# Kernel tuning notes

Measured on AMD Instinct MI355X. Metric: run time of the kernel, lower is better.

The kernel has to match this reference:

```python
import jax, jax.numpy as jnp
import numpy as np

N = 100000; E = 1600000; F = 128; H = 64; LH = 32; K = 10

def setup_inputs():
    key = jax.random.key(0)
    ks = jax.random.split(key, 26)
    p = lambda k, s: jax.random.normal(k, s, dtype=jnp.float32) * 0.05
    return {
        'x': jax.random.normal(ks[0], (N, F), dtype=jnp.float32),
        'edge_index': jax.random.randint(ks[1], (2, E), 0, N, dtype=jnp.int32),
        'W1': p(ks[2], (F, H)), 'b1': p(ks[3], (H,)),
        'W2': p(ks[4], (H, H)), 'b2': p(ks[5], (H,)),
        'W3': p(ks[6], (H, H)), 'b3': p(ks[7], (H,)),
        'Wih0': p(ks[8], (4 * LH, H)), 'Whh0': p(ks[9], (4 * LH, LH)),
        'bih0': p(ks[10], (4 * LH,)), 'bhh0': p(ks[11], (4 * LH,)),
        'Wih1': p(ks[12], (4 * LH, LH)), 'Whh1': p(ks[13], (4 * LH, LH)),
        'bih1': p(ks[14], (4 * LH,)), 'bhh1': p(ks[15], (4 * LH,)),
        'Wv1': p(ks[16], (LH, H // 2)), 'bv1': p(ks[17], (H // 2,)),
        'Wv2': p(ks[18], (H // 2, 1)), 'bv2': p(ks[19], (1,)),
        'Wt1': p(ks[20], (LH, H // 2)), 'bt1': p(ks[21], (H // 2,)),
        'Wt2': p(ks[22], (H // 2, K)), 'bt2': p(ks[23], (K,)),
    }


def _forward(x, edge_index, W1, b1, W2, b2, W3, b3, Wih0, Whh0, bih0, bhh0, Wih1, Whh1, bih1, bhh1, Wv1, bv1, Wv2, bv2, Wt1, bt1, Wt2, bt2):
    n = x.shape[0]
    loops = jnp.arange(n, dtype=edge_index.dtype)
    # PyG GCNConv default: add self-loops, symmetric normalization
    src = jnp.concatenate([edge_index[0], loops])
    dst = jnp.concatenate([edge_index[1], loops])
    deg = jax.ops.segment_sum(jnp.ones_like(src, dtype=x.dtype), dst, num_segments=n)
    dinv = jnp.where(deg > 0, jax.lax.rsqrt(deg), 0.0)
    norm = (dinv[src] * dinv[dst])[:, None]  # D^-1/2 (A+I) D^-1/2 edge weights

    def gcn(h, W, b):
        h = h @ W                                    # transform first (fewer bytes moved)
        agg = jax.ops.segment_sum(h[src] * norm, dst, num_segments=n)
        return agg + b

    h = jax.nn.relu(gcn(x, W1, b1))   # dropout is identity in eval mode
    h = jax.nn.relu(gcn(h, W2, b2))
    h = jax.nn.relu(gcn(h, W3, b3))

    def lstm_step(inp, Wih, Whh, bih, bhh):
        # seq_len == 1 and h0 = c0 = 0 -> recurrent matmul (Whh @ h0) is zero
        g = inp @ Wih.T + bih + bhh
        i, f, gg, o = jnp.split(g, 4, axis=-1)  # torch gate order: i, f, g, o
        c = jax.nn.sigmoid(i) * jnp.tanh(gg)
        return jax.nn.sigmoid(o) * jnp.tanh(c)

    h = lstm_step(h, Wih0, Whh0, bih0, bhh0)
    h = lstm_step(h, Wih1, Whh1, bih1, bhh1)

    volume_pred = jax.nn.relu(h @ Wv1 + bv1) @ Wv2 + bv2
    type_pred = jax.nn.relu(h @ Wt1 + bt1) @ Wt2 + bt2
    return (volume_pred, type_pred)


def reference(x, edge_index, W1, b1, W2, b2, W3, b3, Wih0, Whh0, bih0, bhh0, Wih1, Whh1, bih1, bhh1, Wv1, bv1, Wv2, bv2, Wt1, bt1, Wt2, bt2):
    return _forward(x, edge_index, W1, b1, W2, b2, W3, b3, Wih0, Whh0, bih0, bhh0, Wih1, Whh1, bih1, bhh1, Wv1, bv1, Wv2, bv2, Wt1, bt1, Wt2, bt2)
```

## Files before the change

### kernel.cpp

```cpp
#include <hip/hip_runtime.h>
#include <math.h>


typedef unsigned int  u32;
typedef unsigned short u16;
typedef short bfrag  __attribute__((ext_vector_type(8)));
typedef float f32x4  __attribute__((ext_vector_type(4)));

#define LOG2E 1.44269504088896f
static __device__ __forceinline__ float fast_sigmoid(float x){
  float t = __builtin_amdgcn_exp2f(-x * LOG2E);
  return __builtin_amdgcn_rcpf(1.f + t);
}
static __device__ __forceinline__ float fast_tanh(float x){
  float t = __builtin_amdgcn_exp2f(x * (2.f * LOG2E));
  return 1.f - 2.f * __builtin_amdgcn_rcpf(t + 1.f);
}
static __device__ __forceinline__ float bf2f(u16 u){ return __uint_as_float(((u32)u)<<16); }
static __device__ __forceinline__ u16   f2bf(float f){
  u32 x = __float_as_uint(f);
  return (u16)((x + 0x7fffu + ((x>>16)&1u)) >> 16);
}

#define MAXBK 512

__global__ __launch_bounds__(512) void bucket_hist_kernel(const int* __restrict__ dstA,
                                                          int* __restrict__ bhist, int E){
  __shared__ int h[MAXBK];
  for (int i=threadIdx.x; i<MAXBK; i+=512) h[i]=0;
  __syncthreads();
  const int base = blockIdx.x*8192;
  #pragma unroll
  for (int j=0;j<16;++j){
    int e = base + j*512 + threadIdx.x;
    if (e < E) atomicAdd(&h[dstA[e]>>8], 1);
  }
  __syncthreads();
  for (int i=threadIdx.x; i<MAXBK; i+=512) if (h[i]) atomicAdd(&bhist[i], h[i]);
}

__global__ __launch_bounds__(512) void bucket_scan_kernel(const int* __restrict__ bhist,
                                                          int* __restrict__ bcur,
                                                          int* __restrict__ bstart){
  __shared__ int ts[MAXBK];
  int v = bhist[threadIdx.x];
  ts[threadIdx.x] = v; __syncthreads();
  for (int off=1; off<MAXBK; off<<=1){
    int t = (threadIdx.x>=off) ? ts[threadIdx.x-off] : 0;
    __syncthreads();
    ts[threadIdx.x] += t;
    __syncthreads();
  }
  int ex = ts[threadIdx.x] - v;
  bcur[threadIdx.x]   = ex;
  bstart[threadIdx.x] = ex;
  if (threadIdx.x == MAXBK-1) bstart[MAXBK] = ts[threadIdx.x];
}

__global__ __launch_bounds__(512) void bin_kernel(const int* __restrict__ srcA,
                                                  const int* __restrict__ dstA,
                                                  int* __restrict__ bcur,
                                                  u32* __restrict__ packed, int E){
  __shared__ int h[MAXBK];
  __shared__ int basev[MAXBK];
  for (int i=threadIdx.x; i<MAXBK; i+=512) h[i]=0;
  __syncthreads();
  const int base = blockIdx.x*8192;
  int br[16]; int dv[16];
  #pragma unroll
  for (int j=0;j<16;++j){
    int e = base + j*512 + threadIdx.x;
    if (e < E){
      int d = dstA[e]; int b = d>>8;
      int r = atomicAdd(&h[b], 1);
      br[j] = (b<<16) | r;
      dv[j] = d;
    } else br[j] = -1;
  }
  __syncthreads();
  for (int i=threadIdx.x; i<MAXBK; i+=512){
    int c = h[i];
    basev[i] = c ? atomicAdd(&bcur[i], c) : 0;
  }
  __syncthreads();
  #pragma unroll
  for (int j=0;j<16;++j){
    if (br[j] >= 0){
      int e = base + j*512 + threadIdx.x;
      int pos = basev[br[j]>>16] + (br[j] & 0xffff);
      packed[pos] = (u32)srcA[e] | ((u32)(dv[j] & 255) << 24);
    }
  }
}

__global__ __launch_bounds__(512) void bucket_finalize_kernel(
    const u32* __restrict__ packed, const int* __restrict__ bstart,
    int* __restrict__ offs, float* __restrict__ dinv,
    int* __restrict__ csr, int n, int E){
  __shared__ int cnt[256];
  __shared__ int sc[256];
  __shared__ int cur[256];
  const int b = blockIdx.x;
  const int start = bstart[b], end = bstart[b+1];
  for (int i=threadIdx.x; i<256; i+=512){ cnt[i]=0; cur[i]=0; }
  __syncthreads();
  for (int e = start + threadIdx.x; e < end; e += 512)
    atomicAdd(&cnt[packed[e] >> 24], 1);
  __syncthreads();
  if (threadIdx.x < 256) sc[threadIdx.x] = cnt[threadIdx.x];
  __syncthreads();
  for (int off=1; off<256; off<<=1){
    int t = 0;
    if (threadIdx.x < 256 && threadIdx.x >= off) t = sc[threadIdx.x-off];
    __syncthreads();
    if (threadIdx.x < 256) sc[threadIdx.x] += t;
    __syncthreads();
  }
  if (threadIdx.x < 256){
    int ex = sc[threadIdx.x] - cnt[threadIdx.x];
    sc[threadIdx.x] = ex;
    int node = b*256 + threadIdx.x;
    if (node < n){
      offs[node] = start + ex;
      dinv[node] = rsqrtf((float)(cnt[threadIdx.x] + 1));
    }
  }
  if (b == 0 && threadIdx.x == 0) offs[n] = E;
  __syncthreads();
  for (int e = start + threadIdx.x; e < end; e += 512){
    u32 v = packed[e];
    int loc = v >> 24;
    int pos = start + sc[loc] + atomicAdd(&cur[loc], 1);
    csr[pos] = (int)(v & 0xFFFFFFu);
  }
}

__global__ void count_kernel(const int* __restrict__ dsts, int* __restrict__ deg, int E){
  int e = blockIdx.x*256 + threadIdx.x;
  if (e < E) atomicAdd(&deg[dsts[e]], 1);
}
__global__ void fill_kernel(const int* __restrict__ ei, int* __restrict__ cursor,
                            int* __restrict__ csr, int E){
  int e = blockIdx.x*256 + threadIdx.x;
  if (e < E){
    int d = ei[E + e];
    int pos = atomicAdd(&cursor[d], 1);
    csr[pos] = ei[e];
  }
}

__global__ void scan_reduce_kernel(const int* __restrict__ deg, int* __restrict__ bsums, int n){
  __shared__ int sd[256];
  int base = blockIdx.x*1024 + threadIdx.x*4;
  int s = 0;
  #pragma unroll
  for (int j=0;j<4;++j){ int idx=base+j; if (idx<n) s += deg[idx]; }
  sd[threadIdx.x] = s; __syncthreads();
  for (int off=128; off>0; off>>=1){
    if (threadIdx.x < off) sd[threadIdx.x] += sd[threadIdx.x+off];
    __syncthreads();
  }
  if (threadIdx.x==0) bsums[blockIdx.x] = sd[0];
}

__global__ void scan_block_kernel(const int* __restrict__ bsums, int* __restrict__ boffs, int nb){
  __shared__ int ts[128];
  if (nb <= 128){
    int v = (threadIdx.x < nb) ? bsums[threadIdx.x] : 0;
    ts[threadIdx.x] = v; __syncthreads();
    for (int off=1; off<128; off<<=1){
      int t = (threadIdx.x>=off) ? ts[threadIdx.x-off] : 0;
      __syncthreads();
      ts[threadIdx.x] += t;
      __syncthreads();
    }
    if (threadIdx.x < nb) boffs[threadIdx.x] = ts[threadIdx.x] - v;
  } else if (threadIdx.x==0){
    int run=0;
    for (int b=0;b<nb;++b){ int t=bsums[b]; boffs[b]=run; run+=t; }
  }
}

__global__ void scan_final_kernel(const int* __restrict__ deg, const int* __restrict__ boffs,
                                  int* __restrict__ offs, int n, int E){
  __shared__ int ts[256];
  int base = blockIdx.x*1024 + threadIdx.x*4;
  int v[4]; int s=0;
  #pragma unroll
  for (int j=0;j<4;++j){ int idx=base+j; v[j] = (idx<n) ? deg[idx] : 0; s += v[j]; }
  ts[threadIdx.x] = s; __syncthreads();
  for (int off=1; off<256; off<<=1){
    int t = (threadIdx.x>=off) ? ts[threadIdx.x-off] : 0;
    __syncthreads();
    ts[threadIdx.x] += t;
    __syncthreads();
  }
  int excl = boffs[blockIdx.x] + (threadIdx.x ? ts[threadIdx.x-1] : 0);
  #pragma unroll
  for (int j=0;j<4;++j){ int idx=base+j; if (idx<n){ offs[idx]=excl; excl+=v[j]; } }
  if (blockIdx.x==0 && threadIdx.x==0) offs[n] = E;
}

__global__ void dinv_kernel(const int* __restrict__ deg, const int* __restrict__ offs,
                            int* __restrict__ cursor, float* __restrict__ dinv, int n){
  int i = blockIdx.x*256 + threadIdx.x;
  if (i < n){
    dinv[i] = rsqrtf((float)(deg[i] + 1));
    cursor[i] = offs[i];
  }
}

__global__ void prep_tail_kernel(const float* __restrict__ Wih0, const float* __restrict__ Wih1,
                                 const float* __restrict__ Wv1,  const float* __restrict__ Wt1,
                                 const float* __restrict__ Wv2,  const float* __restrict__ Wt2,
                                 const float* __restrict__ bih0, const float* __restrict__ bhh0,
                                 const float* __restrict__ bih1, const float* __restrict__ bhh1,
                                 const float* __restrict__ Wg1,  const float* __restrict__ Wg2,
                                 const float* __restrict__ Wg3,
                                 u16* __restrict__ wbuf, float* __restrict__ bbuf,
                                 u16* __restrict__ wgcn, int* __restrict__ bhist){
  int tid = blockIdx.x*256 + threadIdx.x;
  if (tid < 6144){
    int kg = tid / 768, rem = tid % 768;
    int j = rem >> 3, k = kg*8 + (rem & 7);
    int row = (j < 32) ? j : j + 32;
    float w = Wih0[row*64 + k];
    u16 hi = f2bf(w);
    wbuf[tid] = hi;
    wbuf[6144 + tid] = f2bf(w - bf2f(hi));
  } else if (tid < 9216){
    int t = tid - 6144;
    int kg = t / 768, rem = t % 768;
    int j = rem >> 3, k = kg*8 + (rem & 7);
    int row = (j < 32) ? j : j + 32;
    wbuf[12288 + t] = f2bf(Wih1[row*32 + k]);
  } else if (tid < 11264){
    int t = tid - 9216;
    int kg = t / 512, rem = t % 512;
    int j = rem >> 3, k = kg*8 + (rem & 7);
    float v = (j < 32) ? Wv1[k*32 + j] : Wt1[k*32 + (j-32)];
    wbuf[15360 + t] = f2bf(v);
  } else if (tid < 11360){
    int t = tid - 11264;
    int row = (t < 32) ? t : t + 32;
    bbuf[t] = bih0[row] + bhh0[row];
  } else if (tid < 11456){
    int t = tid - 11360;
    int row = (t < 32) ? t : t + 32;
    bbuf[96 + t] = bih1[row] + bhh1[row];
  } else if (tid < 12480){
    int t = tid - 11456;
    int slab = t >> 9, within = t & 511;
    int lane = within >> 3, j = within & 7;
    int cc = lane & 15, gg = lane >> 4;
    float v;
    if (slab == 0) v = (cc == 0) ? Wv2[gg*8 + j] : 0.f;
    else           v = (cc < 10) ? Wt2[(gg*8 + j)*10 + cc] : 0.f;
    wbuf[17408 + slab*512 + within] = f2bf(v);
  } else if (tid < 12992){
    bhist[tid - 12480] = 0;
  } else if (tid < 21184){
    int t = tid - 12992;
    int kg = t >> 9, rem = t & 511;
    int j = rem >> 3, k = kg*8 + (rem & 7);
    wgcn[t] = f2bf(Wg1[k*64 + j]);
  } else if (tid < 25280){
    int t = tid - 21184;
    int kg = t >> 9, rem = t & 511;
    int j = rem >> 3, k = kg*8 + (rem & 7);
    wgcn[8192 + t] = f2bf(Wg2[k*64 + j]);
  } else if (tid < 29376){
    int t = tid - 25280;
    int kg = t >> 9, rem = t & 511;
    int j = rem >> 3, k = kg*8 + (rem & 7);
    wgcn[12288 + t] = f2bf(Wg3[k*64 + j]);
  }
}

template<int KD, typename TIN>
__global__ __launch_bounds__(256) void transform_mfma(const TIN* __restrict__ X,
                                                      const u16* __restrict__ WG,
                                                      const float* __restrict__ dinv,
                                                      u16* __restrict__ Y, int n){
  constexpr int XLD = KD + 8;
  __shared__ u16 Xl[128*XLD];
  __shared__ float Dl[128];
  const int tid  = threadIdx.x;
  const int base = blockIdx.x*128;

  if (tid < 128){
    int nd = base + tid;
    Dl[tid] = (nd < n) ? dinv[nd] : 0.f;
  }
  if constexpr (sizeof(TIN)==4){
    #pragma unroll
    for (int j = 0; j < (128*KD)/1024; ++j){
      int e4   = tid + j*256;
      int elem = e4*4;
      int row  = elem / KD, k = elem % KD;
      int gn   = base + row;
      uint2 w2 = make_uint2(0u, 0u);
      if (gn < n){
        float4 v = ((const float4*)X)[(size_t)gn*(KD/4) + (k>>2)];
        w2.x = (u32)f2bf(v.x) | ((u32)f2bf(v.y)<<16);
        w2.y = (u32)f2bf(v.z) | ((u32)f2bf(v.w)<<16);
      }
      *((uint2*)&Xl[row*XLD + k]) = w2;
    }
  } else {
    #pragma unroll
    for (int j = 0; j < (128*KD)/1024; ++j){
      int e4   = tid + j*256;
      int elem = e4*4;
      int row  = elem / KD, k = elem % KD;
      int gn   = base + row;
      uint2 v = make_uint2(0u, 0u);
      if (gn < n) v = *((const uint2*)(X + (size_t)gn*KD + k));
      *((uint2*)&Xl[row*XLD + k]) = v;
    }
  }

  const int lane = tid & 63, wv = tid >> 6;
  const int c = lane & 15, g = lane >> 4;

  bfrag wf[KD/32][4];
  #pragma unroll
  for (int kk=0; kk<KD/32; ++kk)
    #pragma unroll
    for (int nt=0; nt<4; ++nt)
      wf[kk][nt] = *((const bfrag*)&WG[((kk*4+g)<<9) + ((nt*16+c)<<3)]);

  __syncthreads();

  f32x4 acc[2][4];
  #pragma unroll
  for (int rs=0;rs<2;++rs)
    #pragma unroll
    for (int nt=0;nt<4;++nt)
      acc[rs][nt] = (f32x4){0.f,0.f,0.f,0.f};

  #pragma unroll
  for (int kk=0; kk<KD/32; ++kk){
    bfrag a0 = *((const bfrag*)&Xl[(wv*32      + c)*XLD + kk*32 + g*8]);
    bfrag a1 = *((const bfrag*)&Xl[(wv*32 + 16 + c)*XLD + kk*32 + g*8]);
    #pragma unroll
    for (int nt=0; nt<4; ++nt){
      acc[0][nt] = __builtin_amdgcn_mfma_f32_16x16x32_bf16(a0, wf[kk][nt], acc[0][nt], 0,0,0);
      acc[1][nt] = __builtin_amdgcn_mfma_f32_16x16x32_bf16(a1, wf[kk][nt], acc[1][nt], 0,0,0);
    }
  }

  #pragma unroll
  for (int rs=0;rs<2;++rs){
    int nl0 = wv*32 + rs*16 + g*4;
    #pragma unroll
    for (int r=0;r<4;++r){
      int node = base + nl0 + r;
      if (node < n){
        float dv = Dl[nl0 + r];
        #pragma unroll
        for (int nt=0;nt<4;++nt)
          Y[(size_t)node*64 + nt*16 + c] = f2bf(acc[rs][nt][r] * dv);
      }
    }
  }
}

__global__ void agg_kernel(const u16* __restrict__ Hts, const float* __restrict__ dinv,
                           const int* __restrict__ offs, const int* __restrict__ csr,
                           const float* __restrict__ bias, u16* __restrict__ Hout, int n){
  const int lane = threadIdx.x & 63;
  const int wv   = threadIdx.x >> 6;
  const int s    = lane >> 3;
  const int c8   = lane & 7;
  const int node = blockIdx.x*32 + wv*8 + s;
  if (node >= n) return;
  const uint4* __restrict__ H = (const uint4*)Hts;
  float acc[8];
  #pragma unroll
  for (int i=0;i<8;++i) acc[i]=0.f;
  const int beg = offs[node], end = offs[node+1];

  #define ACC8(v) do{ \
    acc[0] += __uint_as_float((v).x<<16); acc[1] += __uint_as_float((v).x & 0xffff0000u); \
    acc[2] += __uint_as_float((v).y<<16); acc[3] += __uint_as_float((v).y & 0xffff0000u); \
    acc[4] += __uint_as_float((v).z<<16); acc[5] += __uint_as_float((v).z & 0xffff0000u); \
    acc[6] += __uint_as_float((v).w<<16); acc[7] += __uint_as_float((v).w & 0xffff0000u); }while(0)

  int j = beg;
  for (; j + 4 <= end; j += 4){
    int s0 = csr[j], s1 = csr[j+1], s2 = csr[j+2], s3 = csr[j+3];
    uint4 v0 = H[(size_t)s0*8 + c8];
    uint4 v1 = H[(size_t)s1*8 + c8];
    uint4 v2 = H[(size_t)s2*8 + c8];
    uint4 v3 = H[(size_t)s3*8 + c8];
    ACC8(v0); ACC8(v1); ACC8(v2); ACC8(v3);
  }
  for (; j < end; ++j){
    int src = csr[j];
    uint4 v = H[(size_t)src*8 + c8];
    ACC8(v);
  }
  #undef ACC8

  uint4 sv = H[(size_t)node*8 + c8];
  float sf[8];
  sf[0]=__uint_as_float(sv.x<<16); sf[1]=__uint_as_float(sv.x & 0xffff0000u);
  sf[2]=__uint_as_float(sv.y<<16); sf[3]=__uint_as_float(sv.y & 0xffff0000u);
  sf[4]=__uint_as_float(sv.z<<16); sf[5]=__uint_as_float(sv.z & 0xffff0000u);
  sf[6]=__uint_as_float(sv.w<<16); sf[7]=__uint_as_float(sv.w & 0xffff0000u);
  float4 b0 = ((const float4*)bias)[c8*2];
  float4 b1 = ((const float4*)bias)[c8*2+1];
  const float dv = dinv[node];
  float o[8];
  o[0]=fmaxf(fmaf(acc[0]+sf[0],dv,b0.x),0.f); o[1]=fmaxf(fmaf(acc[1]+sf[1],dv,b0.y),0.f);
  o[2]=fmaxf(fmaf(acc[2]+sf[2],dv,b0.z),0.f); o[3]=fmaxf(fmaf(acc[3]+sf[3],dv,b0.w),0.f);
  o[4]=fmaxf(fmaf(acc[4]+sf[4],dv,b1.x),0.f); o[5]=fmaxf(fmaf(acc[5]+sf[5],dv,b1.y),0.f);
  o[6]=fmaxf(fmaf(acc[6]+sf[6],dv,b1.z),0.f); o[7]=fmaxf(fmaf(acc[7]+sf[7],dv,b1.w),0.f);
  uint4 w;
  w.x = (u32)f2bf(o[0]) | ((u32)f2bf(o[1])<<16);
  w.y = (u32)f2bf(o[2]) | ((u32)f2bf(o[3])<<16);
  w.z = (u32)f2bf(o[4]) | ((u32)f2bf(o[5])<<16);
  w.w = (u32)f2bf(o[6]) | ((u32)f2bf(o[7])<<16);
  ((uint4*)Hout)[(size_t)node*8 + c8] = w;
}

__global__ __launch_bounds__(256) void lstm_heads_fused(
    const u16* __restrict__ X,
    const u16* __restrict__ wbuf, const float* __restrict__ bbuf,
    const float* __restrict__ bv1, const float* __restrict__ bv2,
    const float* __restrict__ bt1, const float* __restrict__ bt2,
    float* __restrict__ out, int n)
{
  const u16* W0hi = wbuf;
  const u16* W0lo = wbuf + 6144;
  const u16* W1g  = wbuf + 12288;
  const u16* WHg  = wbuf + 15360;
  const u16* BVg  = wbuf + 17408;
  const u16* BTg  = wbuf + 17920;

  __shared__ u16 Hpool[5120];
  __shared__ u16 VT[4608];
  __shared__ float b0l[96], b1l[96], bv1l[32], bt1l[32], bt2l[10];
  u16* H1hi = Hpool;  u16* H1lo = Hpool + 2560;
  u16* H2hi = Hpool;  u16* H2lo = Hpool + 2560;

  const int tid  = threadIdx.x;
  const int base = blockIdx.x*64;

  if (tid < 96)            b0l[tid] = bbuf[tid];
  else if (tid < 192)      b1l[tid-96] = bbuf[tid];
  else if (tid < 224){ int d=tid-192; bv1l[d]=bv1[d]; }
  else               { int d=tid-224; bt1l[d]=bt1[d]; }
  if (tid < 10) bt2l[tid] = bt2[tid];
  __syncthreads();

  const int lane = tid & 63, wv = tid >> 6;
  const int c = lane & 15, g = lane >> 4;
  const float bv2v = bv2[0];

  {
    int r0 = base + wv*16 + c; if (r0 > n-1) r0 = n-1;
    bfrag a0[2];
    a0[0] = *((const bfrag*)(X + (size_t)r0*64      + g*8));
    a0[1] = *((const bfrag*)(X + (size_t)r0*64 + 32 + g*8));
    f32x4 acc[6];
    #pragma unroll
    for (int nt=0;nt<6;++nt) acc[nt] = (f32x4){0.f,0.f,0.f,0.f};
    #pragma unroll
    for (int kk=0; kk<2; ++kk){
      #pragma unroll
      for (int nt=0; nt<6; ++nt){
        int widx = (kk*4+g)*768 + ((nt*16+c)<<3);
        bfrag bh = *((const bfrag*)&W0hi[widx]);
        bfrag bl = *((const bfrag*)&W0lo[widx]);
        acc[nt] = __builtin_amdgcn_mfma_f32_16x16x32_bf16(a0[kk], bh, acc[nt], 0,0,0);
        acc[nt] = __builtin_amdgcn_mfma_f32_16x16x32_bf16(a0[kk], bl, acc[nt], 0,0,0);
      }
    }
    #pragma unroll
    for (int r=0;r<4;++r){
      int rl = wv*16 + g*4 + r;
      #pragma unroll
      for (int half=0; half<2; ++half){
        float iv = acc[0+half][r] + b0l[half*16 + c];
        float gv = acc[2+half][r] + b0l[32 + half*16 + c];
        float ov = acc[4+half][r] + b0l[64 + half*16 + c];
        float cc = fast_sigmoid(iv) * fast_tanh(gv);
        float hv = fast_sigmoid(ov) * fast_tanh(cc);
        u16 hi = f2bf(hv);
        H1hi[rl*40 + half*16 + c] = hi;
        H1lo[rl*40 + half*16 + c] = f2bf(hv - bf2f(hi));
      }
    }
  }
  __syncthreads();

  {
    bfrag w1f[6];
    #pragma unroll
    for (int nt=0; nt<6; ++nt)
      w1f[nt] = *((const bfrag*)&W1g[g*768 + ((nt*16+c)<<3)]);
    bfrag ah = *((const bfrag*)&H1hi[(wv*16 + c)*40 + g*8]);
    bfrag al = *((const bfrag*)&H1lo[(wv*16 + c)*40 + g*8]);
    f32x4 acc[6];
    #pragma unroll
    for (int nt=0;nt<6;++nt) acc[nt] = (f32x4){0.f,0.f,0.f,0.f};
    #pragma unroll
    for (int nt=0; nt<6; ++nt){
      acc[nt] = __builtin_amdgcn_mfma_f32_16x16x32_bf16(ah, w1f[nt], acc[nt], 0,0,0);
      acc[nt] = __builtin_amdgcn_mfma_f32_16x16x32_bf16(al, w1f[nt], acc[nt], 0,0,0);
    }
    __syncthreads();
    #pragma unroll
    for (int r=0;r<4;++r){
      int rl = wv*16 + g*4 + r;
      #pragma unroll
      for (int half=0; half<2; ++half){
        float iv = acc[0+half][r] + b1l[half*16 + c];
        float gv = acc[2+half][r] + b1l[32 + half*16 + c];
        float ov = acc[4+half][r] + b1l[64 + half*16 + c];
        float cc = fast_sigmoid(iv) * fast_tanh(gv);
        float hv = fast_sigmoid(ov) * fast_tanh(cc);
        u16 hi = f2bf(hv);
        H2hi[rl*40 + half*16 + c] = hi;
        H2lo[rl*40 + half*16 + c] = f2bf(hv - bf2f(hi));
      }
    }
  }
  __syncthreads();

  {
    bfrag whf[4];
    #pragma unroll
    for (int nt=0; nt<4; ++nt)
      whf[nt] = *((const bfrag*)&WHg[g*512 + ((nt*16+c)<<3)]);
    bfrag ah = *((const bfrag*)&H2hi[(wv*16 + c)*40 + g*8]);
    bfrag al = *((const bfrag*)&H2lo[(wv*16 + c)*40 + g*8]);
    f32x4 acc[4];
    #pragma unroll
    for (int nt=0;nt<4;++nt) acc[nt] = (f32x4){0.f,0.f,0.f,0.f};
    #pragma unroll
    for (int nt=0; nt<4; ++nt){
      acc[nt] = __builtin_amdgcn_mfma_f32_16x16x32_bf16(ah, whf[nt], acc[nt], 0,0,0);
      acc[nt] = __builtin_amdgcn_mfma_f32_16x16x32_bf16(al, whf[nt], acc[nt], 0,0,0);
    }
    #pragma unroll
    for (int r=0;r<4;++r){
      int rl = wv*16 + g*4 + r;
      VT[rl*72      + c] = f2bf(fmaxf(acc[0][r] + bv1l[c],    0.f));
      VT[rl*72 + 16 + c] = f2bf(fmaxf(acc[1][r] + bv1l[c+16], 0.f));
      VT[rl*72 + 32 + c] = f2bf(fmaxf(acc[2][r] + bt1l[c],    0.f));
      VT[rl*72 + 48 + c] = f2bf(fmaxf(acc[3][r] + bt1l[c+16], 0.f));
    }
  }
  __syncthreads();

  {
    bfrag av = *((const bfrag*)&VT[(wv*16 + c)*72      + g*8]);
    bfrag at = *((const bfrag*)&VT[(wv*16 + c)*72 + 32 + g*8]);
    bfrag bv = *((const bfrag*)(BVg + lane*8));
    bfrag bt = *((const bfrag*)(BTg + lane*8));
    f32x4 accv = (f32x4){0.f,0.f,0.f,0.f};
    f32x4 acct = (f32x4){0.f,0.f,0.f,0.f};
    accv = __builtin_amdgcn_mfma_f32_16x16x32_bf16(av, bv, accv, 0,0,0);
    acct = __builtin_amdgcn_mfma_f32_16x16x32_bf16(at, bt, acct, 0,0,0);
    #pragma unroll
    for (int r=0;r<4;++r){
      int node = base + wv*16 + g*4 + r;
      if (node < n){
        if (c == 0)  out[node] = accv[r] + bv2v;
        if (c < 10)  out[n + (size_t)node*10 + c] = acct[r] + bt2l[c];
      }
    }
  }
}

extern "C" void kernel_launch(void* const* d_in, const int* in_sizes, int n_in,
                              void* d_out, int out_size, void* d_ws, size_t ws_size,
                              hipStream_t stream){
  const float* x    = (const float*)d_in[0];
  const int*   ei   = (const int*)  d_in[1];
  const float* W1   = (const float*)d_in[2];  const float* b1   = (const float*)d_in[3];
  const float* W2   = (const float*)d_in[4];  const float* b2   = (const float*)d_in[5];
  const float* W3   = (const float*)d_in[6];  const float* b3   = (const float*)d_in[7];
  const float* Wih0 = (const float*)d_in[8];
  const float* bih0 = (const float*)d_in[10]; const float* bhh0 = (const float*)d_in[11];
  const float* Wih1 = (const float*)d_in[12];
  const float* bih1 = (const float*)d_in[14]; const float* bhh1 = (const float*)d_in[15];
  const float* Wv1  = (const float*)d_in[16]; const float* bv1  = (const float*)d_in[17];
  const float* Wv2  = (const float*)d_in[18]; const float* bv2  = (const float*)d_in[19];
  const float* Wt1  = (const float*)d_in[20]; const float* bt1  = (const float*)d_in[21];
  const float* Wt2  = (const float*)d_in[22]; const float* bt2  = (const float*)d_in[23];

  const int N  = in_sizes[0] / 128;
  const int E  = in_sizes[1] / 2;
  const int NB = (N + 1023) / 1024;
  const int EB = (E + 8191) / 8192;

  char* w = (char*)d_ws;
  auto take = [&](size_t bytes)->char*{ char* p = w; w += (bytes + 255) & ~(size_t)255; return p; };
  int*   deg    = (int*)  take((size_t)N*4);
  int*   offs   = (int*)  take((size_t)(N+1)*4);
  int*   cursor = (int*)  take((size_t)N*4);
  int*   csr    = (int*)  take((size_t)E*4);
  float* dinv   = (float*)take((size_t)N*4);
  int*   bsums  = (int*)  take((size_t)NB*4);
  int*   boffs  = (int*)  take((size_t)NB*4);
  int*   bhist  = (int*)  take((size_t)MAXBK*4);
  int*   bcur   = (int*)  take((size_t)MAXBK*4);
  int*   bstart = (int*)  take((size_t)(MAXBK+1)*4);
  u32*   packed = (u32*)  take((size_t)E*4);
  u16*   wbuf   = (u16*)  take((size_t)18432*2);
  float* bbuf   = (float*)take((size_t)192*4);
  u16*   wgcn   = (u16*)  take((size_t)16384*2);
  u16*   bufTS  = (u16*)  take((size_t)N*64*2);
  u16*   bufH   = (u16*)  take((size_t)N*64*2);
  (void)ws_size; (void)n_in; (void)out_size;

  prep_tail_kernel<<<115, 256, 0, stream>>>(Wih0, Wih1, Wv1, Wt1, Wv2, Wt2,
                                            bih0, bhh0, bih1, bhh1,
                                            W1, W2, W3,
                                            wbuf, bbuf, wgcn, bhist);

  if (N <= MAXBK*256){
    const int NBK = (N + 255) / 256;
    bucket_hist_kernel    <<<EB,  512, 0, stream>>>(ei + E, bhist, E);
    bucket_scan_kernel    <<<1,   512, 0, stream>>>(bhist, bcur, bstart);
    bin_kernel            <<<EB,  512, 0, stream>>>(ei, ei + E, bcur, packed, E);
    bucket_finalize_kernel<<<NBK, 512, 0, stream>>>(packed, bstart, offs, dinv, csr, N, E);
  } else {
    hipMemsetAsync(deg, 0, (size_t)N*4, stream);
    count_kernel      <<<(E+255)/256, 256, 0, stream>>>(ei + E, deg, E);
    scan_reduce_kernel<<<NB,          256, 0, stream>>>(deg, bsums, N);
    scan_block_kernel <<<1,           128, 0, stream>>>(bsums, boffs, NB);
    scan_final_kernel <<<NB,          256, 0, stream>>>(deg, boffs, offs, N, E);
    dinv_kernel       <<<(N+255)/256, 256, 0, stream>>>(deg, offs, cursor, dinv, N);
    fill_kernel       <<<(E+255)/256, 256, 0, stream>>>(ei, cursor, csr, E);
  }

  const int TB  = (N + 127) / 128;
  const int AB  = (N + 31) / 32;
  transform_mfma<128,float><<<TB, 256, 0, stream>>>(x,    wgcn,         dinv, bufTS, N);
  agg_kernel               <<<AB, 256, 0, stream>>>(bufTS, dinv, offs, csr, b1, bufH, N);
  transform_mfma<64,u16>   <<<TB, 256, 0, stream>>>(bufH, wgcn + 8192,  dinv, bufTS, N);
  agg_kernel               <<<AB, 256, 0, stream>>>(bufTS, dinv, offs, csr, b2, bufH, N);
  transform_mfma<64,u16>   <<<TB, 256, 0, stream>>>(bufH, wgcn + 12288, dinv, bufTS, N);
  agg_kernel               <<<AB, 256, 0, stream>>>(bufTS, dinv, offs, csr, b3, bufH, N);

  const int TB2 = (N + 63) / 64;
  lstm_heads_fused<<<TB2, 256, 0, stream>>>(bufH, wbuf, bbuf,
                                            bv1, bv2, bt1, bt2,
                                            (float*)d_out, N);
}
```

Measured before the change: 200.0 us.

## Fuse GCN aggregation into following transform and LSTM tail kernels

Each aggregation pass now runs as the first phase of the next transform kernel: a block gathers its neighbour rows into shared memory, then applies the MFMA transform directly. The final aggregation is fused into the LSTM/heads kernel the same way. This drops three kernel launches and the write and re-read of the intermediate N×64 bf16 activations. The tradeoff is larger per-block shared memory, and the gather and MFMA phases now serialize within a block, which may reduce occupancy and latency hiding for the irregular gather.

Result: faster. 189.8 us (-5.1%).

```diff
diff --git a/kernel.cpp b/kernel.cpp
--- a/kernel.cpp
+++ b/kernel.cpp
@@ -277,116 +277,21 @@
   }
 }
 
-template<int KD, typename TIN>
-__global__ __launch_bounds__(256) void transform_mfma(const TIN* __restrict__ X,
-                                                      const u16* __restrict__ WG,
-                                                      const float* __restrict__ dinv,
-                                                      u16* __restrict__ Y, int n){
-  constexpr int XLD = KD + 8;
-  __shared__ u16 Xl[128*XLD];
-  __shared__ float Dl[128];
-  const int tid  = threadIdx.x;
-  const int base = blockIdx.x*128;
-
-  if (tid < 128){
-    int nd = base + tid;
-    Dl[tid] = (nd < n) ? dinv[nd] : 0.f;
-  }
-  if constexpr (sizeof(TIN)==4){
-    #pragma unroll
-    for (int j = 0; j < (128*KD)/1024; ++j){
-      int e4   = tid + j*256;
-      int elem = e4*4;
-      int row  = elem / KD, k = elem % KD;
-      int gn   = base + row;
-      uint2 w2 = make_uint2(0u, 0u);
-      if (gn < n){
-        float4 v = ((const float4*)X)[(size_t)gn*(KD/4) + (k>>2)];
-        w2.x = (u32)f2bf(v.x) | ((u32)f2bf(v.y)<<16);
-        w2.y = (u32)f2bf(v.z) | ((u32)f2bf(v.w)<<16);
-      }
-      *((uint2*)&Xl[row*XLD + k]) = w2;
-    }
-  } else {
-    #pragma unroll
-    for (int j = 0; j < (128*KD)/1024; ++j){
-      int e4   = tid + j*256;
-      int elem = e4*4;
-      int row  = elem / KD, k = elem % KD;
-      int gn   = base + row;
-      uint2 v = make_uint2(0u, 0u);
-      if (gn < n) v = *((const uint2*)(X + (size_t)gn*KD + k));
-      *((uint2*)&Xl[row*XLD + k]) = v;
-    }
-  }
-
-  const int lane = tid & 63, wv = tid >> 6;
-  const int c = lane & 15, g = lane >> 4;
-
-  bfrag wf[KD/32][4];
-  #pragma unroll
-  for (int kk=0; kk<KD/32; ++kk)
-    #pragma unroll
-    for (int nt=0; nt<4; ++nt)
-      wf[kk][nt] = *((const bfrag*)&WG[((kk*4+g)<<9) + ((nt*16+c)<<3)]);
-
-  __syncthreads();
-
-  f32x4 acc[2][4];
-  #pragma unroll
-  for (int rs=0;rs<2;++rs)
-    #pragma unroll
-    for (int nt=0;nt<4;++nt)
-      acc[rs][nt] = (f32x4){0.f,0.f,0.f,0.f};
-
-  #pragma unroll
-  for (int kk=0; kk<KD/32; ++kk){
-    bfrag a0 = *((const bfrag*)&Xl[(wv*32      + c)*XLD + kk*32 + g*8]);
-    bfrag a1 = *((const bfrag*)&Xl[(wv*32 + 16 + c)*XLD + kk*32 + g*8]);
-    #pragma unroll
-    for (int nt=0; nt<4; ++nt){
-      acc[0][nt] = __builtin_amdgcn_mfma_f32_16x16x32_bf16(a0, wf[kk][nt], acc[0][nt], 0,0,0);
-      acc[1][nt] = __builtin_amdgcn_mfma_f32_16x16x32_bf16(a1, wf[kk][nt], acc[1][nt], 0,0,0);
-    }
-  }
-
-  #pragma unroll
-  for (int rs=0;rs<2;++rs){
-    int nl0 = wv*32 + rs*16 + g*4;
-    #pragma unroll
-    for (int r=0;r<4;++r){
-      int node = base + nl0 + r;
-      if (node < n){
-        float dv = Dl[nl0 + r];
-        #pragma unroll
-        for (int nt=0;nt<4;++nt)
-          Y[(size_t)node*64 + nt*16 + c] = f2bf(acc[rs][nt][r] * dv);
-      }
-    }
-  }
-}
-
-__global__ void agg_kernel(const u16* __restrict__ Hts, const float* __restrict__ dinv,
-                           const int* __restrict__ offs, const int* __restrict__ csr,
-                           const float* __restrict__ bias, u16* __restrict__ Hout, int n){
-  const int lane = threadIdx.x & 63;
-  const int wv   = threadIdx.x >> 6;
-  const int s    = lane >> 3;
-  const int c8   = lane & 7;
-  const int node = blockIdx.x*32 + wv*8 + s;
-  if (node >= n) return;
-  const uint4* __restrict__ H = (const uint4*)Hts;
+static __device__ __forceinline__ uint4 agg_row(const uint4* __restrict__ H,
+                                                const float* __restrict__ dinv,
+                                                const int* __restrict__ offs,
+                                                const int* __restrict__ csr,
+                                                const float* __restrict__ bias,
+                                                int node, int c8){
   float acc[8];
   #pragma unroll
   for (int i=0;i<8;++i) acc[i]=0.f;
   const int beg = offs[node], end = offs[node+1];
-
   #define ACC8(v) do{ \
     acc[0] += __uint_as_float((v).x<<16); acc[1] += __uint_as_float((v).x & 0xffff0000u); \
     acc[2] += __uint_as_float((v).y<<16); acc[3] += __uint_as_float((v).y & 0xffff0000u); \
     acc[4] += __uint_as_float((v).z<<16); acc[5] += __uint_as_float((v).z & 0xffff0000u); \
     acc[6] += __uint_as_float((v).w<<16); acc[7] += __uint_as_float((v).w & 0xffff0000u); }while(0)
-
   int j = beg;
   for (; j + 4 <= end; j += 4){
     int s0 = csr[j], s1 = csr[j+1], s2 = csr[j+2], s3 = csr[j+3];
@@ -402,7 +307,6 @@
     ACC8(v);
   }
   #undef ACC8
-
   uint4 sv = H[(size_t)node*8 + c8];
   float sf[8];
   sf[0]=__uint_as_float(sv.x<<16); sf[1]=__uint_as_float(sv.x & 0xffff0000u);
@@ -422,11 +326,177 @@
   w.y = (u32)f2bf(o[2]) | ((u32)f2bf(o[3])<<16);
   w.z = (u32)f2bf(o[4]) | ((u32)f2bf(o[5])<<16);
   w.w = (u32)f2bf(o[6]) | ((u32)f2bf(o[7])<<16);
-  ((uint4*)Hout)[(size_t)node*8 + c8] = w;
-}
-
-__global__ __launch_bounds__(256) void lstm_heads_fused(
-    const u16* __restrict__ X,
+  return w;
+}
+
+template<int KD, typename TIN>
+__global__ __launch_bounds__(256) void transform_mfma(const TIN* __restrict__ X,
+                                                      const u16* __restrict__ WG,
+                                                      const float* __restrict__ dinv,
+                                                      u16* __restrict__ Y, int n){
+  constexpr int XLD = KD + 8;
+  __shared__ u16 Xl[128*XLD];
+  __shared__ float Dl[128];
+  const int tid  = threadIdx.x;
+  const int base = blockIdx.x*128;
+
+  if (tid < 128){
+    int nd = base + tid;
+    Dl[tid] = (nd < n) ? dinv[nd] : 0.f;
+  }
+  if constexpr (sizeof(TIN)==4){
+    #pragma unroll
+    for (int j = 0; j < (128*KD)/1024; ++j){
+      int e4   = tid + j*256;
+      int elem = e4*4;
+      int row  = elem / KD, k = elem % KD;
+      int gn   = base + row;
+      uint2 w2 = make_uint2(0u, 0u);
+      if (gn < n){
+        float4 v = ((const float4*)X)[(size_t)gn*(KD/4) + (k>>2)];
+        w2.x = (u32)f2bf(v.x) | ((u32)f2bf(v.y)<<16);
+        w2.y = (u32)f2bf(v.z) | ((u32)f2bf(v.w)<<16);
+      }
+      *((uint2*)&Xl[row*XLD + k]) = w2;
+    }
+  } else {
+    #pragma unroll
+    for (int j = 0; j < (128*KD)/1024; ++j){
+      int e4   = tid + j*256;
+      int elem = e4*4;
+      int row  = elem / KD, k = elem % KD;
+      int gn   = base + row;
+      uint2 v = make_uint2(0u, 0u);
+      if (gn < n) v = *((const uint2*)(X + (size_t)gn*KD + k));
+      *((uint2*)&Xl[row*XLD + k]) = v;
+    }
+  }
+
+  const int lane = tid & 63, wv = tid >> 6;
+  const int c = lane & 15, g = lane >> 4;
+
+  bfrag wf[KD/32][4];
+  #pragma unroll
+  for (int kk=0; kk<KD/32; ++kk)
+    #pragma unroll
+    for (int nt=0; nt<4; ++nt)
+      wf[kk][nt] = *((const bfrag*)&WG[((kk*4+g)<<9) + ((nt*16+c)<<3)]);
+
+  __syncthreads();
+
+  f32x4 acc[2][4];
+  #pragma unroll
+  for (int rs=0;rs<2;++rs)
+    #pragma unroll
+    for (int nt=0;nt<4;++nt)
+      acc[rs][nt] = (f32x4){0.f,0.f,0.f,0.f};
+
+  #pragma unroll
+  for (int kk=0; kk<KD/32; ++kk){
+    bfrag a0 = *((const bfrag*)&Xl[(wv*32      + c)*XLD + kk*32 + g*8]);
+    bfrag a1 = *((const bfrag*)&Xl[(wv*32 + 16 + c)*XLD + kk*32 + g*8]);
+    #pragma unroll
+    for (int nt=0; nt<4; ++nt){
+      acc[0][nt] = __builtin_amdgcn_mfma_f32_16x16x32_bf16(a0, wf[kk][nt], acc[0][nt], 0,0,0);
+      acc[1][nt] = __builtin_amdgcn_mfma_f32_16x16x32_bf16(a1, wf[kk][nt], acc[1][nt], 0,0,0);
+    }
+  }
+
+  #pragma unroll
+  for (int rs=0;rs<2;++rs){
+    int nl0 = wv*32 + rs*16 + g*4;
+    #pragma unroll
+    for (int r=0;r<4;++r){
+      int node = base + nl0 + r;
+      if (node < n){
+        float dv = Dl[nl0 + r];
+        #pragma unroll
+        for (int nt=0;nt<4;++nt)
+          Y[(size_t)node*64 + nt*16 + c] = f2bf(acc[rs][nt][r] * dv);
+      }
+    }
+  }
+}
+
+__global__ __launch_bounds__(256) void fused_agg_transform(
+    const u16* __restrict__ Hsrc, const float* __restrict__ dinv,
+    const int* __restrict__ offs, const int* __restrict__ csr,
+    const float* __restrict__ bias, const u16* __restrict__ WG,
+    u16* __restrict__ Y, int n){
+  constexpr int XLD = 72;
+  __shared__ u16 Xl[128*XLD];
+  __shared__ float Dl[128];
+  const int tid  = threadIdx.x;
+  const int base = blockIdx.x*128;
+  const int lane = tid & 63, wv = tid >> 6;
+
+  if (tid < 128){
+    int nd = base + tid;
+    Dl[tid] = (nd < n) ? dinv[nd] : 0.f;
+  }
+
+  {
+    const int s  = lane >> 3;
+    const int c8 = lane & 7;
+    const uint4* __restrict__ H = (const uint4*)Hsrc;
+    #pragma unroll
+    for (int it=0; it<4; ++it){
+      int rl   = it*32 + wv*8 + s;
+      int node = base + rl;
+      uint4 w = make_uint4(0u,0u,0u,0u);
+      if (node < n) w = agg_row(H, dinv, offs, csr, bias, node, c8);
+      ((uint4*)&Xl[rl*XLD])[c8] = w;
+    }
+  }
+
+  const int c = lane & 15, g = lane >> 4;
+  bfrag wf[2][4];
+  #pragma unroll
+  for (int kk=0; kk<2; ++kk)
+    #pragma unroll
+    for (int nt=0; nt<4; ++nt)
+      wf[kk][nt] = *((const bfrag*)&WG[((kk*4+g)<<9) + ((nt*16+c)<<3)]);
+
+  __syncthreads();
+
+  f32x4 acc[2][4];
+  #pragma unroll
+  for (int rs=0;rs<2;++rs)
+    #pragma unroll
+    for (int nt=0;nt<4;++nt)
+      acc[rs][nt] = (f32x4){0.f,0.f,0.f,0.f};
+
+  #pragma unroll
+  for (int kk=0; kk<2; ++kk){
+    bfrag a0 = *((const bfrag*)&Xl[(wv*32      + c)*XLD + kk*32 + g*8]);
+    bfrag a1 = *((const bfrag*)&Xl[(wv*32 + 16 + c)*XLD + kk*32 + g*8]);
+    #pragma unroll
+    for (int nt=0; nt<4; ++nt){
+      acc[0][nt] = __builtin_amdgcn_mfma_f32_16x16x32_bf16(a0, wf[kk][nt], acc[0][nt], 0,0,0);
+      acc[1][nt] = __builtin_amdgcn_mfma_f32_16x16x32_bf16(a1, wf[kk][nt], acc[1][nt], 0,0,0);
+    }
+  }
+
+  #pragma unroll
+  for (int rs=0;rs<2;++rs){
+    int nl0 = wv*32 + rs*16 + g*4;
+    #pragma unroll
+    for (int r=0;r<4;++r){
+      int node = base + nl0 + r;
+      if (node < n){
+        float dv = Dl[nl0 + r];
+        #pragma unroll
+        for (int nt=0;nt<4;++nt)
+          Y[(size_t)node*64 + nt*16 + c] = f2bf(acc[rs][nt][r] * dv);
+      }
+    }
+  }
+}
+
+__global__ __launch_bounds__(256) void fused_tail(
+    const u16* __restrict__ Hsrc, const float* __restrict__ dinv,
+    const int* __restrict__ offs, const int* __restrict__ csr,
+    const float* __restrict__ b3,
     const u16* __restrict__ wbuf, const float* __restrict__ bbuf,
     const float* __restrict__ bv1, const float* __restrict__ bv2,
     const float* __restrict__ bt1, const float* __restrict__ bt2,
@@ -439,6 +509,7 @@
   const u16* BVg  = wbuf + 17408;
   const u16* BTg  = wbuf + 17920;
 
+  __shared__ u16 XT[64*72];
   __shared__ u16 Hpool[5120];
   __shared__ u16 VT[4608];
   __shared__ float b0l[96], b1l[96], bv1l[32], bt1l[32], bt2l[10];
@@ -447,23 +518,37 @@
 
   const int tid  = threadIdx.x;
   const int base = blockIdx.x*64;
+  const int lane = tid & 63, wv = tid >> 6;
 
   if (tid < 96)            b0l[tid] = bbuf[tid];
   else if (tid < 192)      b1l[tid-96] = bbuf[tid];
   else if (tid < 224){ int d=tid-192; bv1l[d]=bv1[d]; }
   else               { int d=tid-224; bt1l[d]=bt1[d]; }
   if (tid < 10) bt2l[tid] = bt2[tid];
-  __syncthreads();
-
-  const int lane = tid & 63, wv = tid >> 6;
+
+  {
+    const int s  = lane >> 3;
+    const int c8 = lane & 7;
+    const uint4* __restrict__ H = (const uint4*)Hsrc;
+    #pragma unroll
+    for (int it=0; it<2; ++it){
+      int rl   = it*32 + wv*8 + s;
+      int node = base + rl;
+      uint4 w = make_uint4(0u,0u,0u,0u);
+      if (node < n) w = agg_row(H, dinv, offs, csr, b3, node, c8);
+      ((uint4*)&XT[rl*72])[c8] = w;
+    }
+  }
+  __syncthreads();
+
   const int c = lane & 15, g = lane >> 4;
   const float bv2v = bv2[0];
 
   {
-    int r0 = base + wv*16 + c; if (r0 > n-1) r0 = n-1;
+    int rl0 = wv*16 + c;
     bfrag a0[2];
-    a0[0] = *((const bfrag*)(X + (size_t)r0*64      + g*8));
-    a0[1] = *((const bfrag*)(X + (size_t)r0*64 + 32 + g*8));
+    a0[0] = *((const bfrag*)&XT[rl0*72      + g*8]);
+    a0[1] = *((const bfrag*)&XT[rl0*72 + 32 + g*8]);
     f32x4 acc[6];
     #pragma unroll
     for (int nt=0;nt<6;++nt) acc[nt] = (f32x4){0.f,0.f,0.f,0.f};
@@ -614,8 +699,8 @@
   u16*   wbuf   = (u16*)  take((size_t)18432*2);
   float* bbuf   = (float*)take((size_t)192*4);
   u16*   wgcn   = (u16*)  take((size_t)16384*2);
-  u16*   bufTS  = (u16*)  take((size_t)N*64*2);
-  u16*   bufH   = (u16*)  take((size_t)N*64*2);
+  u16*   bufA   = (u16*)  take((size_t)N*64*2);
+  u16*   bufB   = (u16*)  take((size_t)N*64*2);
   (void)ws_size; (void)n_in; (void)out_size;
 
   prep_tail_kernel<<<115, 256, 0, stream>>>(Wih0, Wih1, Wv1, Wt1, Wv2, Wt2,
@@ -640,16 +725,13 @@
   }
 
   const int TB  = (N + 127) / 128;
-  const int AB  = (N + 31) / 32;
-  transform_mfma<128,float><<<TB, 256, 0, stream>>>(x,    wgcn,         dinv, bufTS, N);
-  agg_kernel               <<<AB, 256, 0, stream>>>(bufTS, dinv, offs, csr, b1, bufH, N);
-  transform_mfma<64,u16>   <<<TB, 256, 0, stream>>>(bufH, wgcn + 8192,  dinv, bufTS, N);
-  agg_kernel               <<<AB, 256, 0, stream>>>(bufTS, dinv, offs, csr, b2, bufH, N);
-  transform_mfma<64,u16>   <<<TB, 256, 0, stream>>>(bufH, wgcn + 12288, dinv, bufTS, N);
-  agg_kernel               <<<AB, 256, 0, stream>>>(bufTS, dinv, offs, csr, b3, bufH, N);
-
   const int TB2 = (N + 63) / 64;
-  lstm_heads_fused<<<TB2, 256, 0, stream>>>(bufH, wbuf, bbuf,
-                                            bv1, bv2, bt1, bt2,
-                                            (float*)d_out, N);
-}
+  transform_mfma<128,float><<<TB, 256, 0, stream>>>(x, wgcn, dinv, bufA, N);
+  fused_agg_transform<<<TB, 256, 0, stream>>>(bufA, dinv, offs, csr, b1,
+                                              wgcn + 8192,  bufB, N);
+  fused_agg_transform<<<TB, 256, 0, stream>>>(bufB, dinv, offs, csr, b2,
+                                              wgcn + 12288, bufA, N);
+  fused_tail<<<TB2, 256, 0, stream>>>(bufA, dinv, offs, csr, b3,
+                                      wbuf, bbuf, bv1, bv2, bt1, bt2,
+                                      (float*)d_out, N);
+}
```
